# Optimization experiments

Measured on AMD Instinct MI355X. Metric: run time of the kernel, lower is better.

## Reference

```python
import jax, jax.numpy as jnp
import numpy as np

T = 4096        # tokens
D = 1024        # input_dim
H = 2048        # expert_hidden_dim
O = 1024        # output_dim
E = 8           # num_experts
K = 2           # top_k


def setup_inputs() -> dict:
    key = jax.random.key(0)
    ks = jax.random.split(key, 7)
    s_in = 1.0 / np.sqrt(D)
    s_h = 1.0 / np.sqrt(H)
    return {
        "x": jax.random.normal(ks[0], (T, D), dtype=jnp.float32),
        "Wg": jax.random.uniform(ks[1], (D, E), jnp.float32, -s_in, s_in),
        "bg": jax.random.uniform(ks[2], (E,), jnp.float32, -s_in, s_in),
        "W1": jax.random.uniform(ks[3], (E, D, H), jnp.float32, -s_in, s_in),
        "b1": jax.random.uniform(ks[4], (E, H), jnp.float32, -s_in, s_in),
        "W2": jax.random.uniform(ks[5], (E, H, O), jnp.float32, -s_h, s_h),
        "b2": jax.random.uniform(ks[6], (E, O), jnp.float32, -s_h, s_h),
    }


def reference(x, Wg, bg, W1, b1, W2, b2):
    # Gating: top-k over expert logits, softmax over the k selected logits.
    logits = x @ Wg + bg                                  # [T, E]
    top_vals, top_idx = jax.lax.top_k(logits, K)          # [T, K]
    gates = jax.nn.softmax(top_vals, axis=-1)             # [T, K]

    # Expert MLPs (Linear -> ReLU -> Linear). Each token is processed by the
    # experts it routes to; since an expert's output on x is route-independent,
    # compute all expert outputs once and gather the selected ones (static
    # shapes, jit-friendly equivalent of the masked dispatch loop).
    h = jax.nn.relu(jnp.einsum('td,edh->eth', x, W1) + b1[:, None, :])  # [E,T,H]
    y = jnp.einsum('eth,eho->eto', h, W2) + b2[:, None, :]              # [E,T,O]

    sel = y[top_idx, jnp.arange(T)[:, None]]              # [T, K, O]
    # Weighted combine (scatter_add over batch_idx == per-token sum over K).
    return jnp.sum(sel * gates[..., None], axis=1)        # [T, O]
```

## Files before the change

### kernel.cpp

```cpp
#include <hip/hip_runtime.h>
#include <math.h>


#define T_TOK 4096
#define DIM   1024
#define HID   2048
#define OUTD  1024
#define NE    8

typedef __bf16 bf16_t;
typedef __bf16 bf16x8 __attribute__((ext_vector_type(8)));
typedef float  f32x4  __attribute__((ext_vector_type(4)));

typedef __attribute__((address_space(3))) void       as3_void;
typedef __attribute__((address_space(1))) const void as1_void;
#define GLDS16(src, dst) \
  __builtin_amdgcn_global_load_lds((as1_void*)(src), (as3_void*)(dst), 16, 0, 0)

#define FENCE() asm volatile("" ::: "memory")
#define BARRIER() do { FENCE(); __builtin_amdgcn_s_barrier(); FENCE(); } while (0)
#define LGKM_WAIT() do { \
    asm volatile("s_waitcnt lgkmcnt(0)" ::: "memory"); \
    __builtin_amdgcn_sched_barrier(0); } while (0)
#define VMW_RING() do { \
    if (wid < 4) asm volatile("s_waitcnt vmcnt(4)" ::: "memory"); \
    else         asm volatile("s_waitcnt vmcnt(3)" ::: "memory"); } while (0)
#define VM_WAIT0() asm volatile("s_waitcnt vmcnt(0)" ::: "memory")

__global__ void k_gate(const float* __restrict__ x, const float* __restrict__ Wg,
                       const float* __restrict__ bg, int* __restrict__ einfo,
                       float2* __restrict__ gpair, bf16_t* __restrict__ xb) {
  int wid  = threadIdx.x >> 6;
  int lane = threadIdx.x & 63;
  int t = blockIdx.x * 4 + wid;

  const float4* xr = (const float4*)(x + (size_t)t * DIM);
  float4 xv4[4];
  float sf[NE];
#pragma unroll
  for (int e = 0; e < NE; ++e) sf[e] = 0.f;

#pragma unroll
  for (int i = 0; i < 4; ++i) {
    int q = lane + 64 * i;
    float4 xv = xr[q];
    xv4[i] = xv;
    int d = q * 4;
#pragma unroll
    for (int c = 0; c < 4; ++c) {
      float xc = (&xv.x)[c];
      const float4* wr = (const float4*)(Wg + (size_t)(d + c) * NE);
      float4 w0 = wr[0], w1 = wr[1];
      sf[0] += xc * w0.x; sf[1] += xc * w0.y;
      sf[2] += xc * w0.z; sf[3] += xc * w0.w;
      sf[4] += xc * w1.x; sf[5] += xc * w1.y;
      sf[6] += xc * w1.z; sf[7] += xc * w1.w;
    }
  }

  ushort4* xbr = (ushort4*)(xb + (size_t)t * DIM);
#pragma unroll
  for (int i = 0; i < 4; ++i) {
    union { bf16_t b[4]; ushort4 u; } cv;
    cv.b[0] = (bf16_t)xv4[i].x; cv.b[1] = (bf16_t)xv4[i].y;
    cv.b[2] = (bf16_t)xv4[i].z; cv.b[3] = (bf16_t)xv4[i].w;
    xbr[lane + 64 * i] = cv.u;
  }

  double s[NE];
#pragma unroll
  for (int e = 0; e < NE; ++e) s[e] = (double)sf[e];
#pragma unroll
  for (int off = 32; off > 0; off >>= 1) {
#pragma unroll
    for (int e = 0; e < NE; ++e) s[e] += __shfl_xor(s[e], off);
  }

  if (lane == 0) {
    double v0 = -1e300, v1 = -1e300;
    int i0 = 0, i1 = 0;
#pragma unroll
    for (int e = 0; e < NE; ++e) {
      double v = s[e] + (double)bg[e];
      if (v > v0)      { v1 = v0; i1 = i0; v0 = v; i0 = e; }
      else if (v > v1) { v1 = v;  i1 = e; }
    }
    float ex = expf((float)(v1 - v0));
    float inv = 1.0f / (1.0f + ex);
    einfo[t] = i0 | (i1 << 8);
    gpair[t] = make_float2(inv, ex * inv);
  }
}

__global__ void k_bin(const int* __restrict__ einfo, const float2* __restrict__ gpair,
                      int* __restrict__ cnt, int* __restrict__ offs,
                      int* __restrict__ elist, float* __restrict__ egate,
                      int* __restrict__ tokrec) {
  __shared__ int scnt[NE];
  int w = threadIdx.x >> 6;
  int lane = threadIdx.x & 63;
  unsigned long long below = (lane == 0) ? 0ull : ((~0ull) >> (64 - lane));
  int base = 0;
  for (int c = 0; c < T_TOK / 64; ++c) {
    int t = c * 64 + lane;
    int ei = einfo[t];
    float2 g = gpair[t];
    int e0 = ei & 0xff, e1 = ei >> 8;
    bool m0 = (e0 == w);
    bool m  = m0 || (e1 == w);
    unsigned long long mask = __ballot(m);
    if (m) {
      int pos = base + (int)__popcll(mask & below);
      elist[w * T_TOK + pos] = t;
      egate[w * T_TOK + pos] = m0 ? g.x : g.y;
      tokrec[2 * t + (m0 ? 0 : 1)] = (w << 16) | pos;
    }
    base += (int)__popcll(mask);
  }
  if (lane == 0) scnt[w] = base;
  __syncthreads();
  if (threadIdx.x == 0) {
    int a = 0;
#pragma unroll
    for (int e = 0; e < NE; ++e) {
      cnt[e] = scnt[e];
      offs[e] = a;
      a += scnt[e];
    }
    offs[NE] = a;
  }
}

__global__ void k_tr(const float* __restrict__ W, bf16_t* __restrict__ Wt,
                     int R, int C) {
  __shared__ float tile[64][68];
  size_t ebase = (size_t)blockIdx.z * R * C;
  int c0 = blockIdx.x * 64, r0 = blockIdx.y * 64;
  int tid = threadIdx.x;
  int ty = tid >> 4, tx = tid & 15;
#pragma unroll
  for (int i = 0; i < 4; ++i) {
    int row = ty + i * 16;
    float4 v = *(const float4*)&W[ebase + (size_t)(r0 + row) * C + c0 + tx * 4];
    *(float4*)&tile[row][tx * 4] = v;
  }
  __syncthreads();
  int oc = tid >> 2, seg = tid & 3;
#pragma unroll
  for (int half = 0; half < 2; ++half) {
    union { bf16_t b[8]; uint4 u; } cv;
#pragma unroll
    for (int r = 0; r < 8; ++r)
      cv.b[r] = (bf16_t)tile[seg * 16 + half * 8 + r][oc];
    *(uint4*)&Wt[ebase + (size_t)(c0 + oc) * R + r0 + seg * 16 + half * 8] = cv.u;
  }
}

#define STAGE_A(TT, HH) do { \
    char* _d = smem + (((TT) & 1) * 24576) + ((HH) * 12288); \
    GLDS16(Abase + offA[HH][0] + (TT) * 128, _d + tid * 16); \
    if (tid < 256) GLDS16(Abase + offA[HH][1] + (TT) * 128, _d + (512 + tid) * 16); \
  } while (0)

#define STAGE_B(TT, HH) do { \
    char* _d = smem + 49152 + (((TT) & 1) * 32768) + ((HH) * 16384); \
    GLDS16(Bbase + offB[HH][0] + (TT) * 128, _d + tid * 16); \
    GLDS16(Bbase + offB[HH][1] + (TT) * 128, _d + (512 + tid) * 16); \
  } while (0)

#define MFMA_Q(AF, BF, AH, BH) \
    _Pragma("unroll") for (int i = 0; i < 3; ++i) \
      _Pragma("unroll") for (int j = 0; j < 2; ++j) \
        _Pragma("unroll") for (int kk = 0; kk < 2; ++kk) \
          acc[(AH) * 3 + i][(BH) * 2 + j] = \
            __builtin_amdgcn_mfma_f32_16x16x32_bf16(AF[i][kk], BF[j][kk], \
                acc[(AH) * 3 + i][(BH) * 2 + j], 0, 0, 0)

#define RD_AF(SL) \
    _Pragma("unroll") for (int i = 0; i < 3; ++i) \
      _Pragma("unroll") for (int kk = 0; kk < 2; ++kk) \
        af[i][kk] = *(const bf16x8*)((SL) + rdA[i][kk])

#define KTILE(TT, NTc) do { \
    const char* _a0 = smem + (((TT) & 1) * 24576); \
    const char* _a1 = smem + (((TT) & 1) * 24576) + 12288; \
    const char* _b0 = smem + 49152 + (((TT) & 1) * 32768); \
    const char* _b1 = smem + 49152 + (((TT) & 1) * 32768) + 16384; \
    bf16x8 af[3][2], bf0[2][2], bf1[2][2]; \
    RD_AF(_a0); \
    _Pragma("unroll") for (int j = 0; j < 2; ++j) \
      _Pragma("unroll") for (int kk = 0; kk < 2; ++kk) { \
        bf0[j][kk] = *(const bf16x8*)(_b0 + rdB[j][kk]); \
        bf1[j][kk] = *(const bf16x8*)(_b1 + rdB[j][kk]); \
      } \
    if ((TT) + 1 < (NTc)) { STAGE_A((TT) + 1, 1); STAGE_B((TT) + 1, 1); } \
    BARRIER(); LGKM_WAIT(); \
    __builtin_amdgcn_s_setprio(1); \
    MFMA_Q(af, bf0, 0, 0); MFMA_Q(af, bf1, 0, 1); \
    __builtin_amdgcn_s_setprio(0); BARRIER(); \
    RD_AF(_a1); \
    if ((TT) + 2 < (NTc)) { STAGE_A((TT) + 2, 0); STAGE_B((TT) + 2, 0); \
      VMW_RING(); } \
    else { VM_WAIT0(); } \
    BARRIER(); LGKM_WAIT(); \
    __builtin_amdgcn_s_setprio(1); \
    MFMA_Q(af, bf0, 1, 0); MFMA_Q(af, bf1, 1, 1); \
    __builtin_amdgcn_s_setprio(0); BARRIER(); \
  } while (0)

__launch_bounds__(512, 2)
__global__ void k_gemm1(const bf16_t* __restrict__ xb, const bf16_t* __restrict__ W1t,
                        const float* __restrict__ b1, const int* __restrict__ cnt,
                        const int* __restrict__ offs, const int* __restrict__ elist,
                        bf16_t* __restrict__ hbuf) {
  const int e = blockIdx.z;
  const int count = cnt[e];
  const int rt = blockIdx.y;
  if (rt * 192 >= count) return;
  const int nt = blockIdx.x;

  __shared__ __align__(16) char smem[114688];

  const int tid = threadIdx.x, lane = tid & 63, wid = tid >> 6;
  const int wm = wid >> 2, wn = wid & 3;
  const int fr = lane & 15, lh = lane >> 4;

  unsigned offA[2][2], offB[2][2];
#pragma unroll
  for (int j = 0; j < 2; ++j) {
    int q = j * 512 + tid;
    int r = q >> 3, sfg = (q & 7) ^ (r & 7);
#pragma unroll
    for (int h = 0; h < 2; ++h) {
      int gr = rt * 192 + h * 96 + r;
      if (gr > count - 1) gr = count - 1;
      int tok = elist[e * T_TOK + gr];
      offA[h][j] = (unsigned)((tok * DIM + sfg * 8) * 2);
      int brow = nt * 256 + h * 128 + r;
      offB[h][j] = (unsigned)(((e * HID + brow) * DIM + sfg * 8) * 2);
    }
  }
  unsigned rdA[3][2], rdB[2][2];
#pragma unroll
  for (int i = 0; i < 3; ++i) {
    int r = wm * 48 + i * 16 + fr;
#pragma unroll
    for (int kk = 0; kk < 2; ++kk)
      rdA[i][kk] = (unsigned)(r * 128 + (((kk * 4 + lh) ^ (r & 7)) * 16));
  }
#pragma unroll
  for (int j = 0; j < 2; ++j) {
    int r = wn * 32 + j * 16 + fr;
#pragma unroll
    for (int kk = 0; kk < 2; ++kk)
      rdB[j][kk] = (unsigned)(r * 128 + (((kk * 4 + lh) ^ (r & 7)) * 16));
  }

  const char* Abase = (const char*)xb;
  const char* Bbase = (const char*)W1t;

  f32x4 acc[6][4];
#pragma unroll
  for (int i = 0; i < 6; ++i)
#pragma unroll
    for (int j = 0; j < 4; ++j) acc[i][j] = (f32x4){0.f, 0.f, 0.f, 0.f};

  const int NT = DIM / 64;
  STAGE_A(0, 0); STAGE_B(0, 0); STAGE_A(0, 1); STAGE_B(0, 1);
  STAGE_A(1, 0); STAGE_B(1, 0);
  VMW_RING();
  BARRIER();

  for (int t = 0; t < NT; ++t) KTILE(t, NT);

  const int hbase = offs[e];
#pragma unroll
  for (int mi = 0; mi < 6; ++mi) {
#pragma unroll
    for (int rr = 0; rr < 4; ++rr) {
      int rowp = rt * 192 + (mi / 3) * 96 + wm * 48 + (mi % 3) * 16 + lh * 4 + rr;
      if (rowp < count) {
        size_t hrow = (size_t)(hbase + rowp) * HID;
#pragma unroll
        for (int nj = 0; nj < 4; ++nj) {
          int col = nt * 256 + (nj >> 1) * 128 + wn * 32 + (nj & 1) * 16 + fr;
          float v = acc[mi][nj][rr] + b1[e * HID + col];
          hbuf[hrow + col] = (bf16_t)(v > 0.f ? v : 0.f);
        }
      }
    }
  }
}

__launch_bounds__(512, 2)
__global__ void k_gemm2(const bf16_t* __restrict__ hbuf, const bf16_t* __restrict__ W2t,
                        const float* __restrict__ b2, const int* __restrict__ cnt,
                        const int* __restrict__ offs, const float* __restrict__ egate,
                        float* __restrict__ y) {
  const int e = blockIdx.z;
  const int count = cnt[e];
  const int rt = blockIdx.y;
  if (rt * 192 >= count) return;
  const int nt = blockIdx.x;

  __shared__ __align__(16) char smem[114688];

  const int tid = threadIdx.x, lane = tid & 63, wid = tid >> 6;
  const int wm = wid >> 2, wn = wid & 3;
  const int fr = lane & 15, lh = lane >> 4;
  const int hbase = offs[e];

  unsigned offA[2][2], offB[2][2];
#pragma unroll
  for (int j = 0; j < 2; ++j) {
    int q = j * 512 + tid;
    int r = q >> 3, sfg = (q & 7) ^ (r & 7);
#pragma unroll
    for (int h = 0; h < 2; ++h) {
      int gr = rt * 192 + h * 96 + r;
      if (gr > count - 1) gr = count - 1;
      offA[h][j] = (unsigned)(((hbase + gr) * HID + sfg * 8) * 2);
      int brow = nt * 256 + h * 128 + r;
      offB[h][j] = (unsigned)(((e * OUTD + brow) * HID + sfg * 8) * 2);
    }
  }
  unsigned rdA[3][2], rdB[2][2];
#pragma unroll
  for (int i = 0; i < 3; ++i) {
    int r = wm * 48 + i * 16 + fr;
#pragma unroll
    for (int kk = 0; kk < 2; ++kk)
      rdA[i][kk] = (unsigned)(r * 128 + (((kk * 4 + lh) ^ (r & 7)) * 16));
  }
#pragma unroll
  for (int j = 0; j < 2; ++j) {
    int r = wn * 32 + j * 16 + fr;
#pragma unroll
    for (int kk = 0; kk < 2; ++kk)
      rdB[j][kk] = (unsigned)(r * 128 + (((kk * 4 + lh) ^ (r & 7)) * 16));
  }

  const char* Abase = (const char*)hbuf;
  const char* Bbase = (const char*)W2t;

  f32x4 acc[6][4];
#pragma unroll
  for (int i = 0; i < 6; ++i)
#pragma unroll
    for (int j = 0; j < 4; ++j) acc[i][j] = (f32x4){0.f, 0.f, 0.f, 0.f};

  const int NT = HID / 64;
  STAGE_A(0, 0); STAGE_B(0, 0); STAGE_A(0, 1); STAGE_B(0, 1);
  STAGE_A(1, 0); STAGE_B(1, 0);
  VMW_RING();
  BARRIER();

  for (int t = 0; t < NT; ++t) KTILE(t, NT);

#pragma unroll
  for (int mi = 0; mi < 6; ++mi) {
#pragma unroll
    for (int rr = 0; rr < 4; ++rr) {
      int rowp = rt * 192 + (mi / 3) * 96 + wm * 48 + (mi % 3) * 16 + lh * 4 + rr;
      if (rowp < count) {
        float gate = egate[e * T_TOK + rowp];
        size_t yrow = (size_t)(hbase + rowp) * OUTD;
#pragma unroll
        for (int nj = 0; nj < 4; ++nj) {
          int col = nt * 256 + (nj >> 1) * 128 + wn * 32 + (nj & 1) * 16 + fr;
          y[yrow + col] = gate * (acc[mi][nj][rr] + b2[e * OUTD + col]);
        }
      }
    }
  }
}

__global__ void k_combine(const float* __restrict__ y, const int* __restrict__ offs,
                          const int* __restrict__ tokrec, float* __restrict__ out) {
  int t = blockIdx.x;
  int r0 = tokrec[2 * t], r1 = tokrec[2 * t + 1];
  int s0 = offs[r0 >> 16] + (r0 & 0xffff);
  int s1 = offs[r1 >> 16] + (r1 & 0xffff);
  const float4* ya = (const float4*)(y + (size_t)s0 * OUTD);
  const float4* yb = (const float4*)(y + (size_t)s1 * OUTD);
  float4* o = (float4*)(out + (size_t)t * OUTD);
  int i = threadIdx.x;
  float4 a = ya[i], b = yb[i];
  o[i] = make_float4(a.x + b.x, a.y + b.y, a.z + b.z, a.w + b.w);
}

extern "C" void kernel_launch(void* const* d_in, const int* in_sizes, int n_in,
                              void* d_out, int out_size, void* d_ws, size_t ws_size,
                              hipStream_t stream) {
  const float* x  = (const float*)d_in[0];
  const float* Wg = (const float*)d_in[1];
  const float* bg = (const float*)d_in[2];
  const float* W1 = (const float*)d_in[3];
  const float* b1 = (const float*)d_in[4];
  const float* W2 = (const float*)d_in[5];
  const float* b2 = (const float*)d_in[6];
  float* out = (float*)d_out;

  char* ws = (char*)d_ws;
  int*    cnt    = (int*)(ws);
  int*    offs   = (int*)(ws + 1024);
  int*    tokrec = (int*)(ws + 4096);
  int*    einfo  = (int*)(ws + 36864);
  float2* gpair  = (float2*)(ws + 53248);
  int*    elist  = (int*)(ws + 131072);
  float*  egate  = (float*)(ws + 262144);
  bf16_t* W1t    = (bf16_t*)(ws + (1u << 20));
  float*  y      = (float*)(ws + (1u << 20));
  bf16_t* W2t    = (bf16_t*)(ws + (1u << 20) + (32u << 20));
  bf16_t* xb     = (bf16_t*)(ws + (1u << 20) + (64u << 20));
  bf16_t* hbuf   = (bf16_t*)(ws + (1u << 20) + (72u << 20));

  k_gate<<<T_TOK / 4, 256, 0, stream>>>(x, Wg, bg, einfo, gpair, xb);
  k_bin<<<1, 512, 0, stream>>>(einfo, gpair, cnt, offs, elist, egate, tokrec);
  k_tr<<<dim3(HID / 64, DIM / 64, NE), 256, 0, stream>>>(W1, W1t, DIM, HID);
  k_tr<<<dim3(OUTD / 64, HID / 64, NE), 256, 0, stream>>>(W2, W2t, HID, OUTD);

  k_gemm1<<<dim3(HID / 256, 22, NE), 512, 0, stream>>>(
      xb, W1t, b1, cnt, offs, elist, hbuf);
  k_gemm2<<<dim3(OUTD / 256, 22, NE), 512, 0, stream>>>(
      hbuf, W2t, b2, cnt, offs, egate, y);
  k_combine<<<T_TOK, 256, 0, stream>>>(y, offs, tokrec, out);
}
```

Before: 208.9 us.

## Merge front kernels, use 12-wave GEMM blocks, fuse combine via atomics

```diff
diff --git a/kernel.cpp b/kernel.cpp
--- a/kernel.cpp
+++ b/kernel.cpp
@@ -23,16 +23,19 @@
     asm volatile("s_waitcnt lgkmcnt(0)" ::: "memory"); \
     __builtin_amdgcn_sched_barrier(0); } while (0)
 #define VMW_RING() do { \
-    if (wid < 4) asm volatile("s_waitcnt vmcnt(4)" ::: "memory"); \
-    else         asm volatile("s_waitcnt vmcnt(3)" ::: "memory"); } while (0)
+    if (wid < 4) asm volatile("s_waitcnt vmcnt(3)" ::: "memory"); \
+    else         asm volatile("s_waitcnt vmcnt(2)" ::: "memory"); } while (0)
 #define VM_WAIT0() asm volatile("s_waitcnt vmcnt(0)" ::: "memory")
 
-__global__ void k_gate(const float* __restrict__ x, const float* __restrict__ Wg,
-                       const float* __restrict__ bg, int* __restrict__ einfo,
-                       float2* __restrict__ gpair, bf16_t* __restrict__ xb) {
+__device__ __forceinline__ void gate_body(int bid, const float* __restrict__ x,
+                                          const float* __restrict__ Wg,
+                                          const float* __restrict__ bg,
+                                          int* __restrict__ einfo,
+                                          float2* __restrict__ gpair,
+                                          bf16_t* __restrict__ xb) {
   int wid  = threadIdx.x >> 6;
   int lane = threadIdx.x & 63;
-  int t = blockIdx.x * 4 + wid;
+  int t = bid * 4 + wid;
 
   const float4* xr = (const float4*)(x + (size_t)t * DIM);
   float4 xv4[4];
@@ -92,10 +95,58 @@
   }
 }
 
+__device__ __forceinline__ void tr_body(const float* __restrict__ W,
+                                        bf16_t* __restrict__ Wt, int R, int C,
+                                        int bx, int by, int e,
+                                        float (*tile)[68]) {
+  size_t ebase = (size_t)e * R * C;
+  int c0 = bx * 64, r0 = by * 64;
+  int tid = threadIdx.x;
+  int ty = tid >> 4, tx = tid & 15;
+#pragma unroll
+  for (int i = 0; i < 4; ++i) {
+    int row = ty + i * 16;
+    float4 v = *(const float4*)&W[ebase + (size_t)(r0 + row) * C + c0 + tx * 4];
+    *(float4*)&tile[row][tx * 4] = v;
+  }
+  __syncthreads();
+  int oc = tid >> 2, seg = tid & 3;
+#pragma unroll
+  for (int half = 0; half < 2; ++half) {
+    union { bf16_t b[8]; uint4 u; } cv;
+#pragma unroll
+    for (int r = 0; r < 8; ++r)
+      cv.b[r] = (bf16_t)tile[seg * 16 + half * 8 + r][oc];
+    *(uint4*)&Wt[ebase + (size_t)(c0 + oc) * R + r0 + seg * 16 + half * 8] = cv.u;
+  }
+}
+
+#define NB_GATE (T_TOK / 4)
+#define NB_TR1  ((HID / 64) * (DIM / 64) * NE)
+#define NB_TR2  ((OUTD / 64) * (HID / 64) * NE)
+__global__ void k_front(const float* __restrict__ x, const float* __restrict__ Wg,
+                        const float* __restrict__ bg, int* __restrict__ einfo,
+                        float2* __restrict__ gpair, bf16_t* __restrict__ xb,
+                        const float* __restrict__ W1, bf16_t* __restrict__ W1t,
+                        const float* __restrict__ W2, bf16_t* __restrict__ W2t) {
+  __shared__ float tile[64][68];
+  int bid = blockIdx.x;
+  if (bid < NB_GATE) {
+    gate_body(bid, x, Wg, bg, einfo, gpair, xb);
+  } else if (bid < NB_GATE + NB_TR1) {
+    int i = bid - NB_GATE;
+    tr_body(W1, W1t, DIM, HID, i % (HID / 64), (i / (HID / 64)) % (DIM / 64),
+            i / ((HID / 64) * (DIM / 64)), tile);
+  } else {
+    int i = bid - NB_GATE - NB_TR1;
+    tr_body(W2, W2t, HID, OUTD, i % (OUTD / 64), (i / (OUTD / 64)) % (HID / 64),
+            i / ((OUTD / 64) * (HID / 64)), tile);
+  }
+}
+
 __global__ void k_bin(const int* __restrict__ einfo, const float2* __restrict__ gpair,
                       int* __restrict__ cnt, int* __restrict__ offs,
-                      int* __restrict__ elist, float* __restrict__ egate,
-                      int* __restrict__ tokrec) {
+                      int* __restrict__ elist, float* __restrict__ egate) {
   __shared__ int scnt[NE];
   int w = threadIdx.x >> 6;
   int lane = threadIdx.x & 63;
@@ -113,7 +164,6 @@
       int pos = base + (int)__popcll(mask & below);
       elist[w * T_TOK + pos] = t;
       egate[w * T_TOK + pos] = m0 ? g.x : g.y;
-      tokrec[2 * t + (m0 ? 0 : 1)] = (w << 16) | pos;
     }
     base += (int)__popcll(mask);
   }
@@ -131,62 +181,35 @@
   }
 }
 
-__global__ void k_tr(const float* __restrict__ W, bf16_t* __restrict__ Wt,
-                     int R, int C) {
-  __shared__ float tile[64][68];
-  size_t ebase = (size_t)blockIdx.z * R * C;
-  int c0 = blockIdx.x * 64, r0 = blockIdx.y * 64;
-  int tid = threadIdx.x;
-  int ty = tid >> 4, tx = tid & 15;
-#pragma unroll
-  for (int i = 0; i < 4; ++i) {
-    int row = ty + i * 16;
-    float4 v = *(const float4*)&W[ebase + (size_t)(r0 + row) * C + c0 + tx * 4];
-    *(float4*)&tile[row][tx * 4] = v;
-  }
-  __syncthreads();
-  int oc = tid >> 2, seg = tid & 3;
-#pragma unroll
-  for (int half = 0; half < 2; ++half) {
-    union { bf16_t b[8]; uint4 u; } cv;
-#pragma unroll
-    for (int r = 0; r < 8; ++r)
-      cv.b[r] = (bf16_t)tile[seg * 16 + half * 8 + r][oc];
-    *(uint4*)&Wt[ebase + (size_t)(c0 + oc) * R + r0 + seg * 16 + half * 8] = cv.u;
-  }
-}
-
 #define STAGE_A(TT, HH) do { \
-    char* _d = smem + (((TT) & 1) * 24576) + ((HH) * 12288); \
-    GLDS16(Abase + offA[HH][0] + (TT) * 128, _d + tid * 16); \
-    if (tid < 256) GLDS16(Abase + offA[HH][1] + (TT) * 128, _d + (512 + tid) * 16); \
+    char* _d = smem + ((((TT) & 1) * 2 + (HH)) * 12288); \
+    GLDS16(Abase + offA[HH] + (TT) * 128, _d + tid * 16); } while (0)
+
+#define STAGE_B(TT, HH) do { \
+    char* _d = smem + 49152 + ((((TT) & 1) * 2 + (HH)) * 16384); \
+    GLDS16(Bbase + offB[HH][0] + (TT) * 128, _d + tid * 16); \
+    if (tid < 256) GLDS16(Bbase + offB[HH][1] + (TT) * 128, _d + (768 + tid) * 16); \
   } while (0)
 
-#define STAGE_B(TT, HH) do { \
-    char* _d = smem + 49152 + (((TT) & 1) * 32768) + ((HH) * 16384); \
-    GLDS16(Bbase + offB[HH][0] + (TT) * 128, _d + tid * 16); \
-    GLDS16(Bbase + offB[HH][1] + (TT) * 128, _d + (512 + tid) * 16); \
-  } while (0)
-
 #define MFMA_Q(AF, BF, AH, BH) \
-    _Pragma("unroll") for (int i = 0; i < 3; ++i) \
+    _Pragma("unroll") for (int i = 0; i < 2; ++i) \
       _Pragma("unroll") for (int j = 0; j < 2; ++j) \
         _Pragma("unroll") for (int kk = 0; kk < 2; ++kk) \
-          acc[(AH) * 3 + i][(BH) * 2 + j] = \
+          acc[(AH) * 2 + i][(BH) * 2 + j] = \
             __builtin_amdgcn_mfma_f32_16x16x32_bf16(AF[i][kk], BF[j][kk], \
-                acc[(AH) * 3 + i][(BH) * 2 + j], 0, 0, 0)
+                acc[(AH) * 2 + i][(BH) * 2 + j], 0, 0, 0)
 
 #define RD_AF(SL) \
-    _Pragma("unroll") for (int i = 0; i < 3; ++i) \
+    _Pragma("unroll") for (int i = 0; i < 2; ++i) \
       _Pragma("unroll") for (int kk = 0; kk < 2; ++kk) \
         af[i][kk] = *(const bf16x8*)((SL) + rdA[i][kk])
 
 #define KTILE(TT, NTc) do { \
-    const char* _a0 = smem + (((TT) & 1) * 24576); \
-    const char* _a1 = smem + (((TT) & 1) * 24576) + 12288; \
-    const char* _b0 = smem + 49152 + (((TT) & 1) * 32768); \
-    const char* _b1 = smem + 49152 + (((TT) & 1) * 32768) + 16384; \
-    bf16x8 af[3][2], bf0[2][2], bf1[2][2]; \
+    const char* _a0 = smem + ((((TT) & 1) * 2 + 0) * 12288); \
+    const char* _a1 = smem + ((((TT) & 1) * 2 + 1) * 12288); \
+    const char* _b0 = smem + 49152 + ((((TT) & 1) * 2 + 0) * 16384); \
+    const char* _b1 = smem + 49152 + ((((TT) & 1) * 2 + 1) * 16384); \
+    bf16x8 af[2][2], bf0[2][2], bf1[2][2]; \
     RD_AF(_a0); \
     _Pragma("unroll") for (int j = 0; j < 2; ++j) \
       _Pragma("unroll") for (int kk = 0; kk < 2; ++kk) { \
@@ -208,7 +231,7 @@
     __builtin_amdgcn_s_setprio(0); BARRIER(); \
   } while (0)
 
-__launch_bounds__(512, 2)
+__launch_bounds__(768, 3)
 __global__ void k_gemm1(const bf16_t* __restrict__ xb, const bf16_t* __restrict__ W1t,
                         const float* __restrict__ b1, const int* __restrict__ cnt,
                         const int* __restrict__ offs, const int* __restrict__ elist,
@@ -225,25 +248,28 @@
   const int wm = wid >> 2, wn = wid & 3;
   const int fr = lane & 15, lh = lane >> 4;
 
-  unsigned offA[2][2], offB[2][2];
-#pragma unroll
-  for (int j = 0; j < 2; ++j) {
-    int q = j * 512 + tid;
-    int r = q >> 3, sfg = (q & 7) ^ (r & 7);
-#pragma unroll
-    for (int h = 0; h < 2; ++h) {
-      int gr = rt * 192 + h * 96 + r;
-      if (gr > count - 1) gr = count - 1;
-      int tok = elist[e * T_TOK + gr];
-      offA[h][j] = (unsigned)((tok * DIM + sfg * 8) * 2);
+  const int arow = tid >> 3;
+  const int asfg = (tid & 7) ^ (arow & 7);
+  unsigned offA[2], offB[2][2];
+#pragma unroll
+  for (int h = 0; h < 2; ++h) {
+    int gr = rt * 192 + h * 96 + arow;
+    if (gr > count - 1) gr = count - 1;
+    int tok = elist[e * T_TOK + gr];
+    offA[h] = (unsigned)((tok * DIM + asfg * 8) * 2);
+#pragma unroll
+    for (int j = 0; j < 2; ++j) {
+      int q = j * 768 + tid;
+      int r = q >> 3, sfg = (q & 7) ^ (r & 7);
       int brow = nt * 256 + h * 128 + r;
       offB[h][j] = (unsigned)(((e * HID + brow) * DIM + sfg * 8) * 2);
     }
   }
-  unsigned rdA[3][2], rdB[2][2];
-#pragma unroll
-  for (int i = 0; i < 3; ++i) {
-    int r = wm * 48 + i * 16 + fr;
+
+  unsigned rdA[2][2], rdB[2][2];
+#pragma unroll
+  for (int i = 0; i < 2; ++i) {
+    int r = wm * 32 + i * 16 + fr;
 #pragma unroll
     for (int kk = 0; kk < 2; ++kk)
       rdA[i][kk] = (unsigned)(r * 128 + (((kk * 4 + lh) ^ (r & 7)) * 16));
@@ -259,9 +285,9 @@
   const char* Abase = (const char*)xb;
   const char* Bbase = (const char*)W1t;
 
-  f32x4 acc[6][4];
-#pragma unroll
-  for (int i = 0; i < 6; ++i)
+  f32x4 acc[4][4];
+#pragma unroll
+  for (int i = 0; i < 4; ++i)
 #pragma unroll
     for (int j = 0; j < 4; ++j) acc[i][j] = (f32x4){0.f, 0.f, 0.f, 0.f};
 
@@ -275,10 +301,10 @@
 
   const int hbase = offs[e];
 #pragma unroll
-  for (int mi = 0; mi < 6; ++mi) {
+  for (int mi = 0; mi < 4; ++mi) {
 #pragma unroll
     for (int rr = 0; rr < 4; ++rr) {
-      int rowp = rt * 192 + (mi / 3) * 96 + wm * 48 + (mi % 3) * 16 + lh * 4 + rr;
+      int rowp = rt * 192 + (mi >> 1) * 96 + wm * 32 + (mi & 1) * 16 + lh * 4 + rr;
       if (rowp < count) {
         size_t hrow = (size_t)(hbase + rowp) * HID;
 #pragma unroll
@@ -292,11 +318,11 @@
   }
 }
 
-__launch_bounds__(512, 2)
+__launch_bounds__(768, 3)
 __global__ void k_gemm2(const bf16_t* __restrict__ hbuf, const bf16_t* __restrict__ W2t,
                         const float* __restrict__ b2, const int* __restrict__ cnt,
-                        const int* __restrict__ offs, const float* __restrict__ egate,
-                        float* __restrict__ y) {
+                        const int* __restrict__ offs, const int* __restrict__ elist,
+                        const float* __restrict__ egate, float* __restrict__ out) {
   const int e = blockIdx.z;
   const int count = cnt[e];
   const int rt = blockIdx.y;
@@ -310,24 +336,27 @@
   const int fr = lane & 15, lh = lane >> 4;
   const int hbase = offs[e];
 
-  unsigned offA[2][2], offB[2][2];
-#pragma unroll
-  for (int j = 0; j < 2; ++j) {
-    int q = j * 512 + tid;
-    int r = q >> 3, sfg = (q & 7) ^ (r & 7);
-#pragma unroll
-    for (int h = 0; h < 2; ++h) {
-      int gr = rt * 192 + h * 96 + r;
-      if (gr > count - 1) gr = count - 1;
-      offA[h][j] = (unsigned)(((hbase + gr) * HID + sfg * 8) * 2);
+  const int arow = tid >> 3;
+  const int asfg = (tid & 7) ^ (arow & 7);
+  unsigned offA[2], offB[2][2];
+#pragma unroll
+  for (int h = 0; h < 2; ++h) {
+    int gr = rt * 192 + h * 96 + arow;
+    if (gr > count - 1) gr = count - 1;
+    offA[h] = (unsigned)(((hbase + gr) * HID + asfg * 8) * 2);
+#pragma unroll
+    for (int j = 0; j < 2; ++j) {
+      int q = j * 768 + tid;
+      int r = q >> 3, sfg = (q & 7) ^ (r & 7);
       int brow = nt * 256 + h * 128 + r;
       offB[h][j] = (unsigned)(((e * OUTD + brow) * HID + sfg * 8) * 2);
     }
   }
-  unsigned rdA[3][2], rdB[2][2];
-#pragma unroll
-  for (int i = 0; i < 3; ++i) {
-    int r = wm * 48 + i * 16 + fr;
+
+  unsigned rdA[2][2], rdB[2][2];
+#pragma unroll
+  for (int i = 0; i < 2; ++i) {
+    int r = wm * 32 + i * 16 + fr;
 #pragma unroll
     for (int kk = 0; kk < 2; ++kk)
       rdA[i][kk] = (unsigned)(r * 128 + (((kk * 4 + lh) ^ (r & 7)) * 16));
@@ -343,9 +372,9 @@
   const char* Abase = (const char*)hbuf;
   const char* Bbase = (const char*)W2t;
 
-  f32x4 acc[6][4];
-#pragma unroll
-  for (int i = 0; i < 6; ++i)
+  f32x4 acc[4][4];
+#pragma unroll
+  for (int i = 0; i < 4; ++i)
 #pragma unroll
     for (int j = 0; j < 4; ++j) acc[i][j] = (f32x4){0.f, 0.f, 0.f, 0.f};
 
@@ -358,35 +387,22 @@
   for (int t = 0; t < NT; ++t) KTILE(t, NT);
 
 #pragma unroll
-  for (int mi = 0; mi < 6; ++mi) {
+  for (int mi = 0; mi < 4; ++mi) {
 #pragma unroll
     for (int rr = 0; rr < 4; ++rr) {
-      int rowp = rt * 192 + (mi / 3) * 96 + wm * 48 + (mi % 3) * 16 + lh * 4 + rr;
+      int rowp = rt * 192 + (mi >> 1) * 96 + wm * 32 + (mi & 1) * 16 + lh * 4 + rr;
       if (rowp < count) {
+        int tokv   = elist[e * T_TOK + rowp];
         float gate = egate[e * T_TOK + rowp];
-        size_t yrow = (size_t)(hbase + rowp) * OUTD;
+        float* orow = out + (size_t)tokv * OUTD;
 #pragma unroll
         for (int nj = 0; nj < 4; ++nj) {
           int col = nt * 256 + (nj >> 1) * 128 + wn * 32 + (nj & 1) * 16 + fr;
-          y[yrow + col] = gate * (acc[mi][nj][rr] + b2[e * OUTD + col]);
+          atomicAdd(&orow[col], gate * (acc[mi][nj][rr] + b2[e * OUTD + col]));
         }
       }
     }
   }
-}
-
-__global__ void k_combine(const float* __restrict__ y, const int* __restrict__ offs,
-                          const int* __restrict__ tokrec, float* __restrict__ out) {
-  int t = blockIdx.x;
-  int r0 = tokrec[2 * t], r1 = tokrec[2 * t + 1];
-  int s0 = offs[r0 >> 16] + (r0 & 0xffff);
-  int s1 = offs[r1 >> 16] + (r1 & 0xffff);
-  const float4* ya = (const float4*)(y + (size_t)s0 * OUTD);
-  const float4* yb = (const float4*)(y + (size_t)s1 * OUTD);
-  float4* o = (float4*)(out + (size_t)t * OUTD);
-  int i = threadIdx.x;
-  float4 a = ya[i], b = yb[i];
-  o[i] = make_float4(a.x + b.x, a.y + b.y, a.z + b.z, a.w + b.w);
 }
 
 extern "C" void kernel_launch(void* const* d_in, const int* in_sizes, int n_in,
@@ -404,25 +420,23 @@
   char* ws = (char*)d_ws;
   int*    cnt    = (int*)(ws);
   int*    offs   = (int*)(ws + 1024);
-  int*    tokrec = (int*)(ws + 4096);
   int*    einfo  = (int*)(ws + 36864);
   float2* gpair  = (float2*)(ws + 53248);
   int*    elist  = (int*)(ws + 131072);
   float*  egate  = (float*)(ws + 262144);
   bf16_t* W1t    = (bf16_t*)(ws + (1u << 20));
-  float*  y      = (float*)(ws + (1u << 20));
   bf16_t* W2t    = (bf16_t*)(ws + (1u << 20) + (32u << 20));
   bf16_t* xb     = (bf16_t*)(ws + (1u << 20) + (64u << 20));
   bf16_t* hbuf   = (bf16_t*)(ws + (1u << 20) + (72u << 20));
 
-  k_gate<<<T_TOK / 4, 256, 0, stream>>>(x, Wg, bg, einfo, gpair, xb);
-  k_bin<<<1, 512, 0, stream>>>(einfo, gpair, cnt, offs, elist, egate, tokrec);
-  k_tr<<<dim3(HID / 64, DIM / 64, NE), 256, 0, stream>>>(W1, W1t, DIM, HID);
-  k_tr<<<dim3(OUTD / 64, HID / 64, NE), 256, 0, stream>>>(W2, W2t, HID, OUTD);
-
-  k_gemm1<<<dim3(HID / 256, 22, NE), 512, 0, stream>>>(
+  hipMemsetAsync(out, 0, (size_t)out_size * sizeof(float), stream);
+
+  k_front<<<NB_GATE + NB_TR1 + NB_TR2, 256, 0, stream>>>(
+      x, Wg, bg, einfo, gpair, xb, W1, W1t, W2, W2t);
+  k_bin<<<1, 512, 0, stream>>>(einfo, gpair, cnt, offs, elist, egate);
+
+  k_gemm1<<<dim3(HID / 256, 22, NE), 768, 0, stream>>>(
       xb, W1t, b1, cnt, offs, elist, hbuf);
-  k_gemm2<<<dim3(OUTD / 256, 22, NE), 512, 0, stream>>>(
-      hbuf, W2t, b2, cnt, offs, egate, y);
-  k_combine<<<T_TOK, 256, 0, stream>>>(y, offs, tokrec, out);
-}
+  k_gemm2<<<dim3(OUTD / 256, 22, NE), 768, 0, stream>>>(
+      hbuf, W2t, b2, cnt, offs, elist, egate, out);
+}
```

After: 216.9 us. 1.04x slower.
